# Kernel optimization log

Hardware: AMD Instinct MI355X
Metric: run time of the kernel (lower is better)

The kernel has to match this reference:

```python
import jax, jax.numpy as jnp
import numpy as np
from jax import lax

EPS = 1e-6
B, C, F, K = 64, 512, 1024, 3

def rmsnorm2d(x, w):
    # normalize over channel dim (axis=1), learnable per-channel scale
    inv = lax.rsqrt(jnp.mean(x * x, axis=1, keepdims=True) + EPS)
    return x * inv * w[None, :, None, None]

def pointwise(x, W, b):
    # 1x1 conv == per-pixel matmul: [B,C,H,F] x [O,C] -> [B,O,H,F]
    return jnp.einsum('bchf,oc->bohf', x, W) + b[None, :, None, None]

def depthwise_band(x, W, b):
    # depthwise conv, kernel (1,K), same padding along freq axis
    y = lax.conv_general_dilated(
        x, W,
        window_strides=(1, 1),
        padding=((0, 0), (K // 2, K // 2)),
        dimension_numbers=('NCHW', 'OIHW', 'NCHW'),
        feature_group_count=C)
    return y + b[None, :, None, None]

def setup_inputs() -> dict:
    key = jax.random.key(0)
    ks = jax.random.split(key, 6)
    s = 0.02
    return {
        'x_t': jax.random.normal(ks[0], (B, C, 1, F), jnp.float32),
        'h_prev': jax.random.normal(ks[1], (B, C, 1, F), jnp.float32),
        'in_norm_w': jnp.ones((C,), jnp.float32),
        'hid_norm_w': jnp.ones((C,), jnp.float32),
        'out_norm_w': jnp.ones((C,), jnp.float32),
        'xW': jax.random.normal(ks[2], (3 * C, C), jnp.float32) * s,
        'xb': jnp.zeros((3 * C,), jnp.float32),
        'hmixW': jax.random.normal(ks[3], (C, 1, 1, K), jnp.float32) * s,
        'hmixb': jnp.zeros((C,), jnp.float32),
        'hW': jax.random.normal(ks[4], (3 * C, C), jnp.float32) * s,
        'hb': jnp.zeros((3 * C,), jnp.float32),
    }

def reference(x_t, h_prev, in_norm_w, hid_norm_w, out_norm_w,
              xW, xb, hmixW, hmixb, hW, hb):
    xg = pointwise(rmsnorm2d(x_t, in_norm_w), xW, xb)            # [B,3C,1,F]
    hg = pointwise(depthwise_band(rmsnorm2d(h_prev, hid_norm_w), hmixW, hmixb), hW, hb)
    xr, xz, xn = jnp.split(xg, 3, axis=1)
    hr, hz, hn = jnp.split(hg, 3, axis=1)
    reset = jax.nn.sigmoid(xr + hr)
    update = jax.nn.sigmoid(xz + hz)
    cand = jnp.tanh(xn + reset * hn)
    h_new = (1.0 - update) * cand + update * h_prev
    return rmsnorm2d(h_new + x_t, out_norm_w)
```

## Files before the change

kernel.cpp:

```cpp
#include <hip/hip_runtime.h>

typedef __attribute__((ext_vector_type(8))) short short8;
typedef __attribute__((ext_vector_type(4))) float f32x4;
typedef __attribute__((ext_vector_type(4))) unsigned short u16x4;
typedef unsigned short u16;
typedef unsigned int u32;

#define EPSV 1e-6f

__device__ __forceinline__ u16 f2bf(float f){
  u32 u = __float_as_uint(f);
  u = u + 0x7fffu + ((u >> 16) & 1u);
  return (u16)(u >> 16);
}
__device__ __forceinline__ float bf2f(u16 h){
  return __uint_as_float(((u32)h) << 16);
}
__device__ __forceinline__ float sigm(float v){ return 1.f/(1.f + __expf(-v)); }
__device__ __forceinline__ float tanh_fast(float g){
  float e = __expf(-2.f*fabsf(g));
  return copysignf((1.f - e)/(1.f + e), g);
}
__device__ __forceinline__ void gload_lds16(const void* g, void* l){
  __builtin_amdgcn_global_load_lds(
      (const __attribute__((address_space(1))) u32*)g,
      (__attribute__((address_space(3))) u32*)l, 16, 0, 0);
}

#define WS_WXB   0u
#define WS_WHB   1572864u
#define WS_CB    3145728u
#define WS_SSQP  3153920u
#define WS_SBF   7348224u
#define WS_NEED  74457088u

#define GG_SMEM  163840

extern "C" __global__ void wprep(const float* __restrict__ xW, const float* __restrict__ hW,
                                 const float* __restrict__ inw, const float* __restrict__ hidw,
                                 const float* __restrict__ xb, const float* __restrict__ hmixb,
                                 const float* __restrict__ hb,
                                 u16* __restrict__ xWb, u16* __restrict__ hWb,
                                 float* __restrict__ cb){
  __shared__ float red[4];
  const int n = blockIdx.x;
  const int tid = threadIdx.x;
  float pb = 0.f;
  for (int k = tid; k < 512; k += 256){
    float xw = xW[n*512 + k], hw = hW[n*512 + k];
    xWb[n*512 + k] = f2bf(xw * inw[k]);
    hWb[n*512 + k] = f2bf(hw * hidw[k]);
    pb += hw * hmixb[k];
  }
  #pragma unroll
  for (int off = 1; off < 64; off <<= 1) pb += __shfl_xor(pb, off);
  if ((tid & 63) == 0) red[tid >> 6] = pb;
  __syncthreads();
  if (tid == 0){
    float dot = red[0] + red[1] + red[2] + red[3];
    if (n < 1024){ cb[n] = xb[n] + hb[n] + dot; }
    else         { cb[n] = xb[n]; cb[n + 512] = hb[n] + dot; }
  }
}

extern "C" __global__ void __launch_bounds__(256)
wbuild(const float* __restrict__ x, const float* __restrict__ h,
       const float* __restrict__ hmixW,
       u16* __restrict__ Ax, u16* __restrict__ Ahm)
{
  __shared__ float tile[32][264];
  __shared__ float invx_s[256];
  __shared__ float invh_s[258];
  __shared__ float hmw_s[1536];

  const int b = blockIdx.y, fc = blockIdx.x;
  const int f0 = fc*256;
  const int t = threadIdx.x;
  const int r = t >> 3, q = t & 7;

  for (int i = t; i < 1536; i += 256) hmw_s[i] = hmixW[i];

  float ssq = 0.f;
  for (int cc = 0; cc < 16; ++cc){
    __syncthreads();
    const float* src = x + ((size_t)(b*512 + cc*32 + r))*1024 + f0;
    #pragma unroll
    for (int i = 0; i < 8; ++i)
      *(f32x4*)&tile[r][q*4 + i*32] = *(const f32x4*)(src + q*4 + i*32);
    __syncthreads();
    float p = 0.f;
    #pragma unroll
    for (int rr = 0; rr < 32; ++rr){ float v = tile[rr][t]; p += v*v; }
    ssq += p;
  }
  invx_s[t] = rsqrtf(ssq*(1.f/512.f) + EPSV);
  for (int cc = 0; cc < 16; ++cc){
    __syncthreads();
    const float* src = x + ((size_t)(b*512 + cc*32 + r))*1024 + f0;
    #pragma unroll
    for (int i = 0; i < 8; ++i)
      *(f32x4*)&tile[r][q*4 + i*32] = *(const f32x4*)(src + q*4 + i*32);
    __syncthreads();
    #pragma unroll
    for (int it = 0; it < 4; ++it){
      int id = it*256 + t;
      int pix = id >> 2, c8 = (id & 3)*8;
      float iv = invx_s[pix];
      short8 pk;
      #pragma unroll
      for (int j = 0; j < 8; ++j) pk[j] = (short)f2bf(tile[c8+j][pix]*iv);
      *(short8*)(Ax + ((size_t)(b*1024 + f0 + pix))*512 + cc*32 + c8) = pk;
    }
  }
  float ssqh = 0.f, ssqL = 0.f, ssqR = 0.f;
  for (int cc = 0; cc < 16; ++cc){
    __syncthreads();
    const float* src = h + ((size_t)(b*512 + cc*32 + r))*1024 + f0;
    #pragma unroll
    for (int i = 0; i < 8; ++i)
      *(f32x4*)&tile[r][q*4 + i*32] = *(const f32x4*)(src + q*4 + i*32);
    if (t < 32){
      tile[t][256] = (f0 > 0) ? h[((size_t)(b*512 + cc*32 + t))*1024 + f0 - 1] : 0.f;
    } else if (t < 64){
      int rr = t - 32;
      tile[rr][257] = (f0 + 256 < 1024) ? h[((size_t)(b*512 + cc*32 + rr))*1024 + f0 + 256] : 0.f;
    }
    __syncthreads();
    float p = 0.f;
    #pragma unroll
    for (int rr = 0; rr < 32; ++rr){ float v = tile[rr][t]; p += v*v; }
    ssqh += p;
    if (t == 0){ float p2=0.f; for (int rr=0; rr<32; ++rr){ float v=tile[rr][256]; p2+=v*v; } ssqL += p2; }
    if (t == 1){ float p2=0.f; for (int rr=0; rr<32; ++rr){ float v=tile[rr][257]; p2+=v*v; } ssqR += p2; }
  }
  invh_s[1 + t] = rsqrtf(ssqh*(1.f/512.f) + EPSV);
  if (t == 0) invh_s[0]   = rsqrtf(ssqL*(1.f/512.f) + EPSV);
  if (t == 1) invh_s[257] = rsqrtf(ssqR*(1.f/512.f) + EPSV);
  for (int cc = 0; cc < 16; ++cc){
    __syncthreads();
    const float* src = h + ((size_t)(b*512 + cc*32 + r))*1024 + f0;
    #pragma unroll
    for (int i = 0; i < 8; ++i)
      *(f32x4*)&tile[r][q*4 + i*32] = *(const f32x4*)(src + q*4 + i*32);
    if (t < 32){
      tile[t][256] = (f0 > 0) ? h[((size_t)(b*512 + cc*32 + t))*1024 + f0 - 1] : 0.f;
    } else if (t < 64){
      int rr = t - 32;
      tile[rr][257] = (f0 + 256 < 1024) ? h[((size_t)(b*512 + cc*32 + rr))*1024 + f0 + 256] : 0.f;
    }
    __syncthreads();
    #pragma unroll
    for (int it = 0; it < 4; ++it){
      int id = it*256 + t;
      int pix = id >> 2, c8 = (id & 3)*8;
      int colL = (pix == 0)   ? 256 : (pix - 1);
      int colR = (pix == 255) ? 257 : (pix + 1);
      float iL = invh_s[pix], iC = invh_s[pix+1], iR = invh_s[pix+2];
      short8 pk;
      #pragma unroll
      for (int j = 0; j < 8; ++j){
        int c = c8 + j;
        int cg = cc*32 + c;
        float v = hmw_s[cg*3+0]*tile[c][colL]*iL
                + hmw_s[cg*3+1]*tile[c][pix ]*iC
                + hmw_s[cg*3+2]*tile[c][colR]*iR;
        pk[j] = (short)f2bf(v);
      }
      *(short8*)(Ahm + ((size_t)(b*1024 + f0 + pix))*512 + cc*32 + c8) = pk;
    }
  }
}

extern "C" __global__ void __launch_bounds__(512, 2)
gemm_gates(const float* __restrict__ x, const float* __restrict__ h,
           const u16* __restrict__ Abase,
           const u16* __restrict__ xWb, const u16* __restrict__ hWb,
           const float* __restrict__ cb,
           float* __restrict__ ssqp, u16* __restrict__ sbf)
{
  extern __shared__ __align__(16) char smem[];
  const int t = threadIdx.x;
  const int bid = blockIdx.x;
  const int swz = (bid & 7)*256 + (bid >> 3);
  const int mh = swz >> 4, ch = swz & 15;
  const int b = mh >> 1, f0 = (mh & 1)*512;
  const int c0 = ch*32;
  const int pixbase = b*1024 + f0;
  const int w = t >> 6, lane = t & 63, li = lane & 15, lg = lane >> 4;

  char* Bbase = smem + 65536;

  auto stageB = [&](const u16* Wsrc){
    #pragma unroll
    for (int i = 0; i < 12; ++i){
      int fi = i*8 + w;
      int kk = fi / 6, rem = fi - kk*6;
      int g = rem >> 1, ct = rem & 1;
      gload_lds16(Wsrc + ((size_t)(g*512 + c0 + ct*16 + li))*512 + kk*32 + lg*8,
                  Bbase + fi*1024);
    }
  };
  auto stageA = [&](const u16* Asrc, int kk, int buf){
    char* adst = smem + buf*32768 + w*4096;
    #pragma unroll
    for (int mf = 0; mf < 4; ++mf){
      gload_lds16(Asrc + ((size_t)(pixbase + w*64 + mf*16 + li))*512 + kk*32 + lg*8,
                  adst + mf*1024);
    }
  };

  f32x4 accr[2][4] = {}, accz[2][4] = {}, accg1[2][4] = {}, accg2[2][4] = {};

  auto kstep = [&](int kk, int buf, f32x4 (&accg)[2][4]){
    const char* ab = smem + buf*32768 + w*4096;
    short8 af[4];
    #pragma unroll
    for (int mf = 0; mf < 4; ++mf)
      af[mf] = *(const short8*)(ab + mf*1024 + lane*16);
    #pragma unroll
    for (int ct = 0; ct < 2; ++ct){
      const char* bb = Bbase + (kk*6 + ct)*1024 + lane*16;
      short8 bf0 = *(const short8*)(bb);
      short8 bf1 = *(const short8*)(bb + 2048);
      short8 bf2 = *(const short8*)(bb + 4096);
      #pragma unroll
      for (int mf = 0; mf < 4; ++mf){
        accr[ct][mf] = __builtin_amdgcn_mfma_f32_16x16x32_bf16(af[mf], bf0, accr[ct][mf], 0,0,0);
        accz[ct][mf] = __builtin_amdgcn_mfma_f32_16x16x32_bf16(af[mf], bf1, accz[ct][mf], 0,0,0);
        accg[ct][mf] = __builtin_amdgcn_mfma_f32_16x16x32_bf16(af[mf], bf2, accg[ct][mf], 0,0,0);
      }
    }
  };

  stageB(xWb);
  stageA(Abase, 0, 0);
  __syncthreads();
  #pragma unroll
  for (int j = 0; j < 16; ++j){
    if (j < 15) stageA(Abase, j + 1, (j + 1) & 1);
    kstep(j, j & 1, accg1);
    if (j < 15){ asm volatile("s_waitcnt vmcnt(0)" ::: "memory"); }
    __builtin_amdgcn_sched_barrier(0);
  }
  __syncthreads();
  const u16* A1 = Abase + 33554432;
  stageB(hWb);
  stageA(A1, 0, 0);
  __syncthreads();
  #pragma unroll
  for (int j = 0; j < 16; ++j){
    if (j < 15) stageA(A1, j + 1, (j + 1) & 1);
    kstep(j, j & 1, accg2);
    if (j < 15){ asm volatile("s_waitcnt vmcnt(0)" ::: "memory"); }
    __builtin_amdgcn_sched_barrier(0);
  }
  __syncthreads();

  float (*stg)[516] = (float(*)[516])smem;
  float ps[4][4] = {};
  #pragma unroll
  for (int ct = 0; ct < 2; ++ct){
    const int c = c0 + ct*16 + li;
    const float cbr = cb[c], cbz = cb[512 + c], xbn = cb[1024 + c], hbn = cb[1536 + c];
    #pragma unroll
    for (int mf = 0; mf < 4; ++mf){
      const int f = f0 + w*64 + mf*16 + lg*4;
      const size_t gidx = ((size_t)(b*512 + c))*1024 + f;
      f32x4 hp = *(const f32x4*)(h + gidx);
      f32x4 xt = *(const f32x4*)(x + gidx);
      f32x4 sv;
      #pragma unroll
      for (int j = 0; j < 4; ++j){
        float rr = sigm(accr[ct][mf][j] + cbr);
        float zz = sigm(accz[ct][mf][j] + cbz);
        float g  = accg1[ct][mf][j] + xbn + rr*(accg2[ct][mf][j] + hbn);
        float th = tanh_fast(g);
        float s  = (1.f - zz)*th + zz*hp[j] + xt[j];
        sv[j] = s;
        ps[mf][j] += s*s;
      }
      *(f32x4*)&stg[ct*16 + li][w*64 + mf*16 + lg*4] = sv;
    }
  }
  #pragma unroll
  for (int off = 1; off < 16; off <<= 1)
    #pragma unroll
    for (int mf = 0; mf < 4; ++mf)
      #pragma unroll
      for (int j = 0; j < 4; ++j)
        ps[mf][j] += __shfl_xor(ps[mf][j], off);
  if (li == 0){
    #pragma unroll
    for (int mf = 0; mf < 4; ++mf){
      f32x4 v; v[0]=ps[mf][0]; v[1]=ps[mf][1]; v[2]=ps[mf][2]; v[3]=ps[mf][3];
      *(f32x4*)(ssqp + (size_t)ch*65536 + pixbase + w*64 + mf*16 + lg*4) = v;
    }
  }
  __syncthreads();
  {
    const int cl = t >> 4, seg = t & 15;
    u16* dst = sbf + ((size_t)(b*512 + c0 + cl))*1024 + f0 + seg*32;
    #pragma unroll
    for (int qq = 0; qq < 2; ++qq){
      f32x4 a0 = *(const f32x4*)&stg[cl][seg*32 + qq*16 + 0];
      f32x4 a1 = *(const f32x4*)&stg[cl][seg*32 + qq*16 + 4];
      f32x4 a2 = *(const f32x4*)&stg[cl][seg*32 + qq*16 + 8];
      f32x4 a3 = *(const f32x4*)&stg[cl][seg*32 + qq*16 + 12];
      short8 p0, p1;
      #pragma unroll
      for (int j = 0; j < 4; ++j){
        p0[j]   = (short)f2bf(a0[j]); p0[j+4] = (short)f2bf(a1[j]);
        p1[j]   = (short)f2bf(a2[j]); p1[j+4] = (short)f2bf(a3[j]);
      }
      *(short8*)(dst + qq*16)     = p0;
      *(short8*)(dst + qq*16 + 8) = p1;
    }
  }
}

extern "C" __global__ void __launch_bounds__(256)
outnorm(const float* __restrict__ ssqp, const u16* __restrict__ sbf,
        const float* __restrict__ outw, float* __restrict__ out)
{
  __shared__ float invf[1024];
  const int b = blockIdx.y, cch = blockIdx.x;
  const int t = threadIdx.x;
  f32x4 acc = {};
  #pragma unroll
  for (int p = 0; p < 16; ++p){
    f32x4 v = *(const f32x4*)(ssqp + (size_t)p*65536 + b*1024 + t*4);
    acc[0]+=v[0]; acc[1]+=v[1]; acc[2]+=v[2]; acc[3]+=v[3];
  }
  f32x4 iv;
  #pragma unroll
  for (int j = 0; j < 4; ++j) iv[j] = rsqrtf(acc[j]*(1.f/512.f) + EPSV);
  *(f32x4*)&invf[t*4] = iv;
  __syncthreads();
  for (int cl = 0; cl < 32; ++cl){
    const int c = cch*32 + cl;
    const float ow = outw[c];
    const u16* row = sbf + ((size_t)(b*512 + c))*1024;
    u16x4 sv = *(const u16x4*)(row + t*4);
    f32x4 o;
    #pragma unroll
    for (int j = 0; j < 4; ++j) o[j] = bf2f(sv[j]) * invf[t*4 + j] * ow;
    *(f32x4*)(out + ((size_t)(b*512 + c))*1024 + t*4) = o;
  }
}

#define FB_AXN_OFF 0
#define FB_AHM_OFF 32768
#define FB_RAW_OFF 65536
#define FB_PART_OFF 102400
#define FB_INVX_OFF 104512
#define FB_INVH_OFF 104640
#define FB_SSQ2_OFF 104784
#define FB_INVO_OFF 105936
#define FB_SMEM_BYTES 106112

extern "C" __global__ void fb_wconv(const float* __restrict__ xW, const float* __restrict__ hW,
                                    u16* __restrict__ xWb, u16* __restrict__ hWb){
  int i = blockIdx.x*256 + threadIdx.x;
  xWb[i] = f2bf(xW[i]);
  hWb[i] = f2bf(hW[i]);
}

extern "C" __global__ void __launch_bounds__(512, 2)
fb_gru(const float* __restrict__ x, const float* __restrict__ h,
       const float* __restrict__ inw, const float* __restrict__ hidw,
       const float* __restrict__ outw,
       const float* __restrict__ xb, const float* __restrict__ hmixWc,
       const float* __restrict__ hmixb, const float* __restrict__ hb,
       const u16* __restrict__ xWb, const u16* __restrict__ hWb,
       float* __restrict__ out)
{
  extern __shared__ __align__(16) char smem[];
  const int b  = blockIdx.y;
  const int f0 = blockIdx.x * 32;
  const int t  = threadIdx.x;
  u16* raw = (u16*)(smem + FB_RAW_OFF);
  float* part = (float*)(smem + FB_PART_OFF);
  {
    const int fq = t & 7, cb2 = t >> 3;
    #pragma unroll
    for (int pass = 0; pass < 8; ++pass){
      int c = pass*64 + cb2;
      f32x4 v = *(const f32x4*)(x + ((size_t)(b*512 + c))*1024 + f0 + fq*4);
      u16* d = raw + c*36 + fq*4;
      d[0] = f2bf(v[0]); d[1] = f2bf(v[1]); d[2] = f2bf(v[2]); d[3] = f2bf(v[3]);
    }
  }
  __syncthreads();
  {
    const int f = t & 31, cs = t >> 5;
    float p = 0.f;
    for (int i = 0; i < 32; ++i){ float v = bf2f(raw[(cs*32 + i)*36 + f]); p += v*v; }
    part[cs*33 + f] = p;
  }
  __syncthreads();
  if (t < 32){
    float s = 0.f;
    for (int i = 0; i < 16; ++i) s += part[i*33 + t];
    ((float*)(smem + FB_INVX_OFF))[t] = rsqrtf(s*(1.f/512.f) + EPSV);
  }
  __syncthreads();
  {
    const int f = t >> 4, cc = t & 15;
    const float iv = ((float*)(smem + FB_INVX_OFF))[f];
    #pragma unroll
    for (int it = 0; it < 4; ++it){
      int cbase = (cc + it*16)*8;
      short8 pk;
      #pragma unroll
      for (int j = 0; j < 8; ++j){
        float v = bf2f(raw[(cbase+j)*36 + f]) * iv * inw[cbase+j];
        pk[j] = (short)f2bf(v);
      }
      *(short8*)(smem + FB_AXN_OFF + f*1024 + ((cbase*2) ^ ((f&7)<<4))) = pk;
    }
  }
  __syncthreads();
  {
    const int fq = t & 7, cb2 = t >> 3;
    #pragma unroll
    for (int pass = 0; pass < 8; ++pass){
      int c = pass*64 + cb2;
      f32x4 v = *(const f32x4*)(h + ((size_t)(b*512 + c))*1024 + f0 + fq*4);
      u16* d = raw + c*36 + 1 + fq*4;
      d[0] = f2bf(v[0]); d[1] = f2bf(v[1]); d[2] = f2bf(v[2]); d[3] = f2bf(v[3]);
    }
    {
      int c = t;
      size_t base = ((size_t)(b*512 + c))*1024;
      float lv = (f0 > 0)          ? h[base + f0 - 1]  : 0.f;
      float rv = (f0 + 32 < 1024)  ? h[base + f0 + 32] : 0.f;
      raw[c*36 + 0]  = f2bf(lv);
      raw[c*36 + 33] = f2bf(rv);
    }
  }
  __syncthreads();
  {
    const int fw = t & 63, cs = t >> 6;
    if (fw < 34){
      float p = 0.f;
      for (int i = 0; i < 64; ++i){ float v = bf2f(raw[(cs*64 + i)*36 + fw]); p += v*v; }
      part[cs*35 + fw] = p;
    }
  }
  __syncthreads();
  if (t < 34){
    float s = 0.f;
    for (int i = 0; i < 8; ++i) s += part[i*35 + t];
    ((float*)(smem + FB_INVH_OFF))[t] = rsqrtf(s*(1.f/512.f) + EPSV);
  }
  __syncthreads();
  {
    const int fr = t >> 5, cc = t & 31;
    const float* invh = (const float*)(smem + FB_INVH_OFF);
    const float iL = invh[fr], iC = invh[fr + 1], iR = invh[fr + 2];
    #pragma unroll
    for (int it = 0; it < 2; ++it){
      const int cbase = (cc + it*32)*8;
      short8 o;
      #pragma unroll
      for (int j = 0; j < 8; ++j){
        int c = cbase + j;
        float hL = bf2f(raw[c*36 + fr])     * iL;
        float hC = bf2f(raw[c*36 + fr + 1]) * iC;
        float hR = bf2f(raw[c*36 + fr + 2]) * iR;
        float v = (hmixWc[c*3]*hL + hmixWc[c*3+1]*hC + hmixWc[c*3+2]*hR) * hidw[c] + hmixb[c];
        o[j] = (short)f2bf(v);
      }
      *(short8*)(smem + FB_AHM_OFF + fr*1024 + ((cbase*2) ^ ((fr&7)<<4))) = o;
    }
  }
  __syncthreads();
  const int wv = t >> 6, lane = t & 63, li = lane & 15, lg = lane >> 4;
  const int n0 = wv*64;
  f32x4 ar[2][4] = {}, az[2][4] = {}, axg[2][4] = {}, ahg[2][4] = {};
  #pragma unroll
  for (int src = 0; src < 2; ++src){
    const char* A = smem + (src ? FB_AHM_OFF : FB_AXN_OFF);
    const u16* W = src ? hWb : xWb;
    for (int k0 = 0; k0 < 512; k0 += 32){
      const int kb = (k0*2 + lg*16) ^ ((li & 7) << 4);
      short8 a0 = *(const short8*)(A + li*1024 + kb);
      short8 a1 = *(const short8*)(A + (li+16)*1024 + kb);
      #pragma unroll
      for (int nt = 0; nt < 4; ++nt){
        const u16* bp = W + (size_t)(n0 + nt*16 + li)*512 + k0 + lg*8;
        short8 br = *(const short8*)(bp);
        short8 bz = *(const short8*)(bp + 512*512);
        short8 bg = *(const short8*)(bp + 1024*512);
        ar[0][nt] = __builtin_amdgcn_mfma_f32_16x16x32_bf16(a0, br, ar[0][nt], 0,0,0);
        ar[1][nt] = __builtin_amdgcn_mfma_f32_16x16x32_bf16(a1, br, ar[1][nt], 0,0,0);
        az[0][nt] = __builtin_amdgcn_mfma_f32_16x16x32_bf16(a0, bz, az[0][nt], 0,0,0);
        az[1][nt] = __builtin_amdgcn_mfma_f32_16x16x32_bf16(a1, bz, az[1][nt], 0,0,0);
        if (src == 0){
          axg[0][nt] = __builtin_amdgcn_mfma_f32_16x16x32_bf16(a0, bg, axg[0][nt], 0,0,0);
          axg[1][nt] = __builtin_amdgcn_mfma_f32_16x16x32_bf16(a1, bg, axg[1][nt], 0,0,0);
        } else {
          ahg[0][nt] = __builtin_amdgcn_mfma_f32_16x16x32_bf16(a0, bg, ahg[0][nt], 0,0,0);
          ahg[1][nt] = __builtin_amdgcn_mfma_f32_16x16x32_bf16(a1, bg, ahg[1][nt], 0,0,0);
        }
      }
    }
  }
  float ps[8] = {0,0,0,0,0,0,0,0};
  #pragma unroll
  for (int nt = 0; nt < 4; ++nt){
    const int c = n0 + nt*16 + li;
    const float xbr = xb[c], xbz = xb[512+c], xbg = xb[1024+c];
    const float hbr = hb[c], hbz = hb[512+c], hbg = hb[1024+c];
    #pragma unroll
    for (int mt = 0; mt < 2; ++mt){
      const size_t idx = ((size_t)(b*512 + c))*1024 + f0 + mt*16 + lg*4;
      const f32x4 hp = *(const f32x4*)(h + idx);
      const f32x4 xt = *(const f32x4*)(x + idx);
      f32x4 sv;
      #pragma unroll
      for (int j = 0; j < 4; ++j){
        float rr = sigm(ar[mt][nt][j] + xbr + hbr);
        float zz = sigm(az[mt][nt][j] + xbz + hbz);
        float g  = axg[mt][nt][j] + xbg + rr*(ahg[mt][nt][j] + hbg);
        float th = tanh_fast(g);
        float hv = (1.f - zz)*th + zz*hp[j];
        float s  = hv + xt[j];
        sv[j] = s;
        ps[mt*4 + j] += s*s;
      }
      ar[mt][nt] = sv;
    }
  }
  #pragma unroll
  for (int off = 1; off < 16; off <<= 1){
    #pragma unroll
    for (int p = 0; p < 8; ++p) ps[p] += __shfl_xor(ps[p], off);
  }
  __syncthreads();
  float* stg = (float*)(smem + FB_AXN_OFF);
  #pragma unroll
  for (int nt = 0; nt < 4; ++nt){
    const int n = n0 + nt*16 + li;
    #pragma unroll
    for (int mt = 0; mt < 2; ++mt){
      const int m0 = mt*16 + lg*4;
      *(f32x4*)(stg + n*32 + (m0 ^ ((n & 7) << 2))) = ar[mt][nt];
    }
  }
  float* sq2 = (float*)(smem + FB_SSQ2_OFF);
  if (li == 0){
    #pragma unroll
    for (int p = 0; p < 8; ++p){
      int m = (p >> 2)*16 + lg*4 + (p & 3);
      sq2[m*9 + wv] = ps[p];
    }
  }
  __syncthreads();
  if (t < 32){
    float s = 0.f;
    for (int i = 0; i < 8; ++i) s += sq2[t*9 + i];
    ((float*)(smem + FB_INVO_OFF))[t] = rsqrtf(s*(1.f/512.f) + EPSV);
  }
  __syncthreads();
  {
    const float* invO = (const float*)(smem + FB_INVO_OFF);
    const int cb2 = t >> 3, chh = t & 7;
    #pragma unroll
    for (int pass = 0; pass < 8; ++pass){
      int c = pass*64 + cb2;
      int base = (chh*4) ^ ((c & 7) << 2);
      f32x4 v = *(const f32x4*)(stg + c*32 + base);
      float ow = outw[c];
      f32x4 o;
      #pragma unroll
      for (int j = 0; j < 4; ++j) o[j] = v[j] * invO[chh*4 + j] * ow;
      *(f32x4*)(out + ((size_t)(b*512 + c))*1024 + f0 + chh*4) = o;
    }
  }
}

extern "C" void kernel_launch(void* const* d_in, const int* in_sizes, int n_in,
                              void* d_out, int out_size, void* d_ws, size_t ws_size,
                              hipStream_t stream){
  (void)in_sizes; (void)n_in; (void)out_size;
  const float* x      = (const float*)d_in[0];
  const float* h      = (const float*)d_in[1];
  const float* inw    = (const float*)d_in[2];
  const float* hidw   = (const float*)d_in[3];
  const float* outw   = (const float*)d_in[4];
  const float* xW     = (const float*)d_in[5];
  const float* xb     = (const float*)d_in[6];
  const float* hmixW  = (const float*)d_in[7];
  const float* hmixb  = (const float*)d_in[8];
  const float* hW     = (const float*)d_in[9];
  const float* hb     = (const float*)d_in[10];

  if (ws_size >= (size_t)WS_NEED){
    u16*   xWb  = (u16*)((char*)d_ws + WS_WXB);
    u16*   hWb  = (u16*)((char*)d_ws + WS_WHB);
    float* cbw  = (float*)((char*)d_ws + WS_CB);
    float* ssqp = (float*)((char*)d_ws + WS_SSQP);
    u16*   sbf  = (u16*)((char*)d_ws + WS_SBF);
    u16*   Ax   = (u16*)d_out;

    hipFuncSetAttribute(reinterpret_cast<const void*>(gemm_gates),
                        hipFuncAttributeMaxDynamicSharedMemorySize, GG_SMEM);

    wprep<<<1536, 256, 0, stream>>>(xW, hW, inw, hidw, xb, hmixb, hb, xWb, hWb, cbw);
    wbuild<<<dim3(4, 64), 256, 0, stream>>>(x, h, hmixW, Ax, Ax + 33554432);
    gemm_gates<<<2048, 512, GG_SMEM, stream>>>(x, h, Ax, xWb, hWb, cbw, ssqp, sbf);
    outnorm<<<dim3(16, 64), 256, 0, stream>>>(ssqp, sbf, outw, (float*)d_out);
  } else {
    u16* xWb = (u16*)d_ws;
    u16* hWb = xWb + 786432;
    hipFuncSetAttribute(reinterpret_cast<const void*>(fb_gru),
                        hipFuncAttributeMaxDynamicSharedMemorySize, FB_SMEM_BYTES);
    fb_wconv<<<3072, 256, 0, stream>>>(xW, hW, xWb, hWb);
    dim3 grid(32, 64);
    fb_gru<<<grid, 512, FB_SMEM_BYTES, stream>>>(x, h, inw, hidw, outw,
                                                 xb, hmixW, hmixb, hb,
                                                 xWb, hWb, (float*)d_out);
  }
}
```

Baseline: 614.5 us.

## Load GEMM A fragments directly into registers and stage x/h epilogue reads through LDS

The A operand is now read straight from global memory into registers with two register buffers for prefetch. This replaces the double-buffered LDS staging, the per-step vmcnt waits and the sched barriers, and frees 64KB of LDS. The epilogue's x_t/h_prev reads were strided per channel row; they are now loaded into LDS with coalesced row-wise copies and then read in MFMA layout. Costs are more register pressure, exposure to global latency with only one k-step of lookahead, and an extra LDS pass in the epilogue.

```diff
diff --git a/kernel.cpp b/kernel.cpp
--- a/kernel.cpp
+++ b/kernel.cpp
@@ -34,7 +34,7 @@
 #define WS_SBF   7348224u
 #define WS_NEED  74457088u
 
-#define GG_SMEM  163840
+#define GG_SMEM  132096
 
 extern "C" __global__ void wprep(const float* __restrict__ xW, const float* __restrict__ hW,
                                  const float* __restrict__ inw, const float* __restrict__ hidw,
@@ -188,7 +188,7 @@
   const int pixbase = b*1024 + f0;
   const int w = t >> 6, lane = t & 63, li = lane & 15, lg = lane >> 4;
 
-  char* Bbase = smem + 65536;
+  char* Bbase = smem;
 
   auto stageB = [&](const u16* Wsrc){
     #pragma unroll
@@ -200,23 +200,16 @@
                   Bbase + fi*1024);
     }
   };
-  auto stageA = [&](const u16* Asrc, int kk, int buf){
-    char* adst = smem + buf*32768 + w*4096;
-    #pragma unroll
-    for (int mf = 0; mf < 4; ++mf){
-      gload_lds16(Asrc + ((size_t)(pixbase + w*64 + mf*16 + li))*512 + kk*32 + lg*8,
-                  adst + mf*1024);
-    }
+  const size_t arow = ((size_t)(pixbase + w*64 + li))*512 + lg*8;
+  auto loadA = [&](const u16* Asrc, int kk, short8 (&dst)[4]){
+    #pragma unroll
+    for (int mf = 0; mf < 4; ++mf)
+      dst[mf] = *(const short8*)(Asrc + arow + (size_t)mf*16*512 + kk*32);
   };
 
   f32x4 accr[2][4] = {}, accz[2][4] = {}, accg1[2][4] = {}, accg2[2][4] = {};
 
-  auto kstep = [&](int kk, int buf, f32x4 (&accg)[2][4]){
-    const char* ab = smem + buf*32768 + w*4096;
-    short8 af[4];
-    #pragma unroll
-    for (int mf = 0; mf < 4; ++mf)
-      af[mf] = *(const short8*)(ab + mf*1024 + lane*16);
+  auto kstepR = [&](int kk, const short8 (&af)[4], f32x4 (&accg)[2][4]){
     #pragma unroll
     for (int ct = 0; ct < 2; ++ct){
       const char* bb = Bbase + (kk*6 + ct)*1024 + lane*16;
@@ -232,31 +225,49 @@
     }
   };
 
+  short8 aE[4], aO[4];
+
   stageB(xWb);
-  stageA(Abase, 0, 0);
-  __syncthreads();
-  #pragma unroll
-  for (int j = 0; j < 16; ++j){
-    if (j < 15) stageA(Abase, j + 1, (j + 1) & 1);
-    kstep(j, j & 1, accg1);
-    if (j < 15){ asm volatile("s_waitcnt vmcnt(0)" ::: "memory"); }
-    __builtin_amdgcn_sched_barrier(0);
+  loadA(Abase, 0, aE);
+  loadA(Abase, 1, aO);
+  __syncthreads();
+  #pragma unroll
+  for (int jj = 0; jj < 8; ++jj){
+    kstepR(2*jj, aE, accg1);
+    if (jj < 7) loadA(Abase, 2*jj + 2, aE);
+    kstepR(2*jj + 1, aO, accg1);
+    if (jj < 7) loadA(Abase, 2*jj + 3, aO);
   }
   __syncthreads();
   const u16* A1 = Abase + 33554432;
   stageB(hWb);
-  stageA(A1, 0, 0);
-  __syncthreads();
-  #pragma unroll
-  for (int j = 0; j < 16; ++j){
-    if (j < 15) stageA(A1, j + 1, (j + 1) & 1);
-    kstep(j, j & 1, accg2);
-    if (j < 15){ asm volatile("s_waitcnt vmcnt(0)" ::: "memory"); }
-    __builtin_amdgcn_sched_barrier(0);
-  }
-  __syncthreads();
-
-  float (*stg)[516] = (float(*)[516])smem;
+  loadA(A1, 0, aE);
+  loadA(A1, 1, aO);
+  __syncthreads();
+  #pragma unroll
+  for (int jj = 0; jj < 8; ++jj){
+    kstepR(2*jj, aE, accg2);
+    if (jj < 7) loadA(A1, 2*jj + 2, aE);
+    kstepR(2*jj + 1, aO, accg2);
+    if (jj < 7) loadA(A1, 2*jj + 3, aO);
+  }
+  __syncthreads();
+
+  float (*stgX)[516] = (float(*)[516])smem;
+  float (*stgH)[516] = (float(*)[516])(smem + 66048);
+  {
+    const int col = (t & 127)*4;
+    const int r0  = t >> 7;
+    #pragma unroll
+    for (int p2 = 0; p2 < 8; ++p2){
+      int row = p2*4 + r0;
+      const size_t g = ((size_t)(b*512 + c0 + row))*1024 + f0 + col;
+      *(f32x4*)&stgX[row][col] = *(const f32x4*)(x + g);
+      *(f32x4*)&stgH[row][col] = *(const f32x4*)(h + g);
+    }
+  }
+  __syncthreads();
+
   float ps[4][4] = {};
   #pragma unroll
   for (int ct = 0; ct < 2; ++ct){
@@ -264,10 +275,9 @@
     const float cbr = cb[c], cbz = cb[512 + c], xbn = cb[1024 + c], hbn = cb[1536 + c];
     #pragma unroll
     for (int mf = 0; mf < 4; ++mf){
-      const int f = f0 + w*64 + mf*16 + lg*4;
-      const size_t gidx = ((size_t)(b*512 + c))*1024 + f;
-      f32x4 hp = *(const f32x4*)(h + gidx);
-      f32x4 xt = *(const f32x4*)(x + gidx);
+      const int fcol = w*64 + mf*16 + lg*4;
+      f32x4 hp = *(const f32x4*)&stgH[ct*16 + li][fcol];
+      f32x4 xt = *(const f32x4*)&stgX[ct*16 + li][fcol];
       f32x4 sv;
       #pragma unroll
       for (int j = 0; j < 4; ++j){
@@ -279,7 +289,7 @@
         sv[j] = s;
         ps[mf][j] += s*s;
       }
-      *(f32x4*)&stg[ct*16 + li][w*64 + mf*16 + lg*4] = sv;
+      *(f32x4*)&stgX[ct*16 + li][fcol] = sv;
     }
   }
   #pragma unroll
@@ -302,10 +312,10 @@
     u16* dst = sbf + ((size_t)(b*512 + c0 + cl))*1024 + f0 + seg*32;
     #pragma unroll
     for (int qq = 0; qq < 2; ++qq){
-      f32x4 a0 = *(const f32x4*)&stg[cl][seg*32 + qq*16 + 0];
-      f32x4 a1 = *(const f32x4*)&stg[cl][seg*32 + qq*16 + 4];
-      f32x4 a2 = *(const f32x4*)&stg[cl][seg*32 + qq*16 + 8];
-      f32x4 a3 = *(const f32x4*)&stg[cl][seg*32 + qq*16 + 12];
+      f32x4 a0 = *(const f32x4*)&stgX[cl][seg*32 + qq*16 + 0];
+      f32x4 a1 = *(const f32x4*)&stgX[cl][seg*32 + qq*16 + 4];
+      f32x4 a2 = *(const f32x4*)&stgX[cl][seg*32 + qq*16 + 8];
+      f32x4 a3 = *(const f32x4*)&stgX[cl][seg*32 + qq*16 + 12];
       short8 p0, p1;
       #pragma unroll
       for (int j = 0; j < 4; ++j){
```

New measurement: 659.5 us. 1.07x slower.
